# Optimization experiments

Measured on AMD Instinct MI355X. Metric: run time of the kernel, lower is better.

## Reference

```python
import jax, jax.numpy as jnp
import numpy as np

B, T, F_IN, H = 128, 512, 128, 128
EPS = 1e-5


def setup_inputs() -> dict:
    key = jax.random.key(0)
    ks = jax.random.split(key, 24)
    s = 0.05
    r = lambda k, shp: jax.random.normal(k, shp, jnp.float32) * s
    return {
        "x": jax.random.normal(ks[0], (B, T, F_IN), jnp.float32),
        "group_labels": jax.random.randint(ks[1], (B,), 0, 4),
        "conv1_w": r(ks[2], (64, F_IN, 3)), "conv1_b": jnp.zeros((64,), jnp.float32),
        "bn1_g": jnp.ones((64,), jnp.float32), "bn1_b": jnp.zeros((64,), jnp.float32),
        "conv2_w": r(ks[3], (128, 64, 3)), "conv2_b": jnp.zeros((128,), jnp.float32),
        "bn2_g": jnp.ones((128,), jnp.float32), "bn2_b": jnp.zeros((128,), jnp.float32),
        "wih0": r(ks[4], (2, 4 * H, 128)), "whh0": r(ks[5], (2, 4 * H, H)), "b0": r(ks[6], (2, 4 * H)),
        "wih1": r(ks[7], (2, 4 * H, 2 * H)), "whh1": r(ks[8], (2, 4 * H, H)), "b1": r(ks[9], (2, 4 * H)),
        "att_w": r(ks[10], (2 * H,)), "att_b": r(ks[11], (1,)),
        "dec_w1": r(ks[12], (4, 64, 2 * H)), "dec_b1": r(ks[13], (4, 64)),
        "dec_w2": r(ks[14], (4, 32, 64)), "dec_b2": r(ks[15], (4, 32)),
        "dec_w3": r(ks[16], (4, 1, 32)), "dec_b3": r(ks[17], (4, 1)),
    }


def _bn(x, g, b):
    # training-mode batch stats over (N, L) per channel; x: (B, C, L)
    m = x.mean(axis=(0, 2), keepdims=True)
    v = x.var(axis=(0, 2), keepdims=True)
    return (x - m) / jnp.sqrt(v + EPS) * g[None, :, None] + b[None, :, None]


def _conv1d(x, w, b):
    # x: (B, C, L), w: (O, I, 3), padding=1
    y = jax.lax.conv_general_dilated(x, w, (1,), ((1, 1),), dimension_numbers=("NCH", "OIH", "NCH"))
    return y + b[None, :, None]


def _lstm_dir(x, wih, whh, b, reverse):
    Bv, Hv = x.shape[0], whh.shape[1]
    xg = jnp.einsum("btd,gd->btg", x, wih) + b  # precomputed input gates (B, T, 4H)

    def step(carry, xt):
        h, c = carry
        gates = xt + h @ whh.T
        i, f, g, o = jnp.split(gates, 4, axis=-1)  # torch gate order i,f,g,o
        c = jax.nn.sigmoid(f) * c + jax.nn.sigmoid(i) * jnp.tanh(g)
        h = jax.nn.sigmoid(o) * jnp.tanh(c)
        return (h, c), h

    init = (jnp.zeros((Bv, Hv), x.dtype), jnp.zeros((Bv, Hv), x.dtype))
    _, hs = jax.lax.scan(step, init, jnp.swapaxes(xg, 0, 1), reverse=reverse)
    return jnp.swapaxes(hs, 0, 1)  # (B, T, H), time-aligned for both directions


def _bilstm(x, wih, whh, b):
    hf = _lstm_dir(x, wih[0], whh[0], b[0], False)
    hb = _lstm_dir(x, wih[1], whh[1], b[1], True)
    return jnp.concatenate([hf, hb], axis=-1)


def reference(x, group_labels, conv1_w, conv1_b, bn1_g, bn1_b, conv2_w, conv2_b,
              bn2_g, bn2_b, wih0, whh0, b0, wih1, whh1, b1, att_w, att_b,
              dec_w1, dec_b1, dec_w2, dec_b2, dec_w3, dec_b3):
    # ---- shared encoder ----
    h = jnp.swapaxes(x, 1, 2)                          # (B, F, T)
    h = jax.nn.relu(_bn(_conv1d(h, conv1_w, conv1_b), bn1_g, bn1_b))
    h = jax.nn.relu(_bn(_conv1d(h, conv2_w, conv2_b), bn2_g, bn2_b))
    h = jnp.swapaxes(h, 1, 2)                          # (B, T, 128)
    h = _bilstm(h, wih0, whh0, b0)                     # (B, T, 2H)
    h = _bilstm(h, wih1, whh1, b1)                     # (B, T, 2H)
    scores = h @ att_w + att_b                         # (B, T)
    attn = jax.nn.softmax(scores, axis=1)
    attended = jnp.einsum("bt,btd->bd", attn, h)       # (B, 2H)
    # ---- group-routed decoders (batch=1 per sample in original => BN skipped) ----
    h1 = jax.nn.relu(jnp.einsum("bd,ehd->beh", attended, dec_w1) + dec_b1[None])   # (B,4,64)
    h2 = jax.nn.relu(jnp.einsum("beh,egh->beg", h1, dec_w2) + dec_b2[None])         # (B,4,32)
    outs = jnp.einsum("beg,eog->beo", h2, dec_w3) + dec_b3[None]                    # (B,4,1)
    preds = jnp.take_along_axis(outs[:, :, 0], group_labels[:, None], axis=1)       # (B,1)
    return preds, attn
```

## Files before the change

### kernel.cpp

```cpp
#include <hip/hip_runtime.h>
#include <hip/hip_bf16.h>

#define EPS_ 1e-5f

typedef __attribute__((ext_vector_type(4))) float f32x4;
typedef __attribute__((ext_vector_type(8))) short s16x8;
typedef __attribute__((ext_vector_type(4))) short s16x4;
typedef unsigned short u16;

static __device__ __forceinline__ u16 f2bf(float f) {
  __hip_bfloat16 h = __float2bfloat16(f);
  return *reinterpret_cast<u16*>(&h);
}
static __device__ __forceinline__ float bf2f(u16 u) {
  union { float f; unsigned int i; } v; v.i = ((unsigned int)u) << 16; return v.f;
}
static __device__ __forceinline__ float sigf(float x) {
  return __builtin_amdgcn_rcpf(1.f + __expf(-x));
}
static __device__ __forceinline__ float tanhf_(float x) {
  return 2.f * __builtin_amdgcn_rcpf(1.f + __expf(-2.f * x)) - 1.f;
}
static __device__ __forceinline__ f32x4 mfma16(s16x8 a, s16x8 b, f32x4 c) {
  return __builtin_amdgcn_mfma_f32_16x16x32_bf16(a, b, c, 0, 0, 0);
}

__global__ void convw_kernel(const float* __restrict__ src, u16* __restrict__ dst,
                             int KIN, int ksbits, int total) {
  int i = blockIdx.x * 256 + threadIdx.x;
  if (i >= total) return;
  int e = i & 7;
  int lane = (i >> 3) & 63;
  int w = (i >> 9) & 7;
  int g = (i >> 12) & 3;
  int t2 = i >> 14;
  int ks = t2 & ((1 << ksbits) - 1);
  int d = t2 >> ksbits;
  int r = g * 128 + w * 16 + (lane & 15);
  int k = ks * 32 + (lane >> 4) * 8 + e;
  dst[i] = f2bf(src[((size_t)d * 512 + r) * KIN + k]);
}

__global__ void convwf_kernel(const float* __restrict__ src, u16* __restrict__ dst,
                              int IC, int NW, int total) {
  int i = blockIdx.x * 256 + threadIdx.x;
  if (i >= total) return;
  int e = i & 7;
  int lane = (i >> 3) & 63;
  int blk = i >> 9;
  int wb = blk % NW;
  int ks = blk / NW;
  int oc = wb * 16 + (lane & 15);
  int k = ks * 32 + (lane >> 4) * 8 + e;
  int tap = k / IC;
  int ic = k - tap * IC;
  dst[i] = f2bf(src[(oc * IC + ic) * 3 + tap]);
}

template<int IC, int NW, bool BN>
__global__ __launch_bounds__(512, 1) void convm_kernel(
    const float* __restrict__ xin, const u16* __restrict__ wP,
    const float* __restrict__ bsrc, const float* __restrict__ stats_in,
    const float* __restrict__ g_in, const float* __restrict__ beta_in,
    float* __restrict__ yout, float* __restrict__ stats_out) {
  constexpr int OC = NW * 16;
  constexpr int NKS = (3 * IC) / 32;
  constexpr int ICQ = IC / 32;
  __shared__ u16 xs[66 * IC];
  __shared__ float insc[IC], insh[IC];

  const int tid = threadIdx.x;
  const int wv = tid >> 6, lane = tid & 63, q = lane >> 4, col = lane & 15;
  const int b = blockIdx.x >> 3;
  const int t0 = (blockIdx.x & 7) * 64;
  char* xsb = (char*)xs;

  if constexpr (BN) {
    for (int c = tid; c < IC; c += 512) {
      float s0 = stats_in[2 * c], s1 = stats_in[2 * c + 1];
      float m = s0 * (1.f / 65536.f);
      float v = s1 * (1.f / 65536.f) - m * m;
      float inv = rsqrtf(v + EPS_);
      float a = g_in[c] * inv;
      insc[c] = a; insh[c] = beta_in[c] - m * a;
    }
    __syncthreads();
  }

  for (int n = tid; n < 66 * (IC / 4); n += 512) {
    int r = n / (IC / 4);
    int c4 = (n % (IC / 4)) * 4;
    int t = t0 + r - 1;
    float v0 = 0.f, v1 = 0.f, v2 = 0.f, v3 = 0.f;
    if (t >= 0 && t < 512) {
      f32x4 v = *(const f32x4*)&xin[((size_t)b * 512 + t) * IC + c4];
      v0 = v[0]; v1 = v[1]; v2 = v[2]; v3 = v[3];
      if constexpr (BN) {
        v0 = fmaxf(v0 * insc[c4 + 0] + insh[c4 + 0], 0.f);
        v1 = fmaxf(v1 * insc[c4 + 1] + insh[c4 + 1], 0.f);
        v2 = fmaxf(v2 * insc[c4 + 2] + insh[c4 + 2], 0.f);
        v3 = fmaxf(v3 * insc[c4 + 3] + insh[c4 + 3], 0.f);
      }
    }
    s16x4 u;
    u[0] = (short)f2bf(v0); u[1] = (short)f2bf(v1);
    u[2] = (short)f2bf(v2); u[3] = (short)f2bf(v3);
    int byte = ((r * IC + c4) * 2) ^ ((r & 7) << 4);
    *(s16x4*)(xsb + byte) = u;
  }
  __syncthreads();

  const int wb = (NW == 8) ? wv : (wv & 3);
  const s16x8* wPv = (const s16x8*)wP;
  s16x8 aA[NKS];
#pragma unroll
  for (int ks = 0; ks < NKS; ++ks)
    aA[ks] = wPv[(ks * NW + wb) * 64 + lane];

  f32x4 bias4 = *(const f32x4*)&bsrc[wb * 16 + q * 4];

  constexpr int NSUB = (NW == 8) ? 4 : 2;
  const int st0 = (NW == 8) ? 0 : ((wv >> 2) * 2);

  float ssum0 = 0.f, ssum1 = 0.f, ssum2 = 0.f, ssum3 = 0.f;
  float ssq0 = 0.f, ssq1 = 0.f, ssq2 = 0.f, ssq3 = 0.f;

#pragma unroll
  for (int s = 0; s < NSUB; ++s) {
    const int tbase = (st0 + s) * 16;
    const int t_loc = tbase + col;
    f32x4 acc = bias4;
#pragma unroll
    for (int ks = 0; ks < NKS; ++ks) {
      const int tap = ks / ICQ;
      const int icb = (ks % ICQ) * 32 + q * 8;
      const int R = t_loc + tap;
      int byte = ((R * IC + icb) * 2) ^ ((R & 7) << 4);
      s16x8 bB = *(const s16x8*)(xsb + byte);
      acc = mfma16(aA[ks], bB, acc);
    }
    *(f32x4*)&yout[((size_t)b * 512 + t0 + t_loc) * OC + wb * 16 + q * 4] = acc;
    ssum0 += acc[0]; ssq0 += acc[0] * acc[0];
    ssum1 += acc[1]; ssq1 += acc[1] * acc[1];
    ssum2 += acc[2]; ssq2 += acc[2] * acc[2];
    ssum3 += acc[3]; ssq3 += acc[3] * acc[3];
  }

#define RED16(S)                                   \
  S += __shfl_xor(S, 1, 64); S += __shfl_xor(S, 2, 64); \
  S += __shfl_xor(S, 4, 64); S += __shfl_xor(S, 8, 64);
  RED16(ssum0) RED16(ssum1) RED16(ssum2) RED16(ssum3)
  RED16(ssq0)  RED16(ssq1)  RED16(ssq2)  RED16(ssq3)
#undef RED16
  if (col == 0) {
    const int ocb = wb * 16 + q * 4;
    atomicAdd(&stats_out[2 * (ocb + 0)], ssum0);
    atomicAdd(&stats_out[2 * (ocb + 0) + 1], ssq0);
    atomicAdd(&stats_out[2 * (ocb + 1)], ssum1);
    atomicAdd(&stats_out[2 * (ocb + 1) + 1], ssq1);
    atomicAdd(&stats_out[2 * (ocb + 2)], ssum2);
    atomicAdd(&stats_out[2 * (ocb + 2) + 1], ssq2);
    atomicAdd(&stats_out[2 * (ocb + 3)], ssum3);
    atomicAdd(&stats_out[2 * (ocb + 3) + 1], ssq3);
  }
}

template<int KIN, bool BN>
__global__ __launch_bounds__(512, 1) void xg_kernel(
    const void* __restrict__ xin_, const float* __restrict__ stats,
    const float* __restrict__ bng, const float* __restrict__ bnb,
    const u16* __restrict__ wihP, const float* __restrict__ bias,
    u16* __restrict__ xgo) {
  constexpr int NKS = KIN / 32;
  constexpr int XSTR = KIN + 8;
  __shared__ u16 xl[2][16][XSTR];
  __shared__ float sc[128], sh[128];

  const int tid = threadIdx.x;
  const int wv = tid >> 6, lane = tid & 63, q = lane >> 4, col = lane & 15;
  const int bid = blockIdx.x;
  const int dir = bid >> 7, bg = (bid >> 4) & 7, t0 = (bid & 15) * 32;
  const int b0 = bg * 16;
  const int ss = tid >> 5, cc = tid & 31;
  const float* xf = (const float*)xin_;
  const u16* xh = (const u16*)xin_;

  if constexpr (BN) {
    for (int c = tid; c < 128; c += 512) {
      float s0 = stats[2 * c], s1 = stats[2 * c + 1];
      float m = s0 * (1.f / 65536.f);
      float v = s1 * (1.f / 65536.f) - m * m;
      float inv = rsqrtf(v + EPS_);
      float a = bng[c] * inv;
      sc[c] = a; sh[c] = bnb[c] - m * a;
    }
    __syncthreads();
  }

  const s16x8* wihv = (const s16x8*)wihP;
  s16x8 aw[NKS][4];
#pragma unroll
  for (int ks = 0; ks < NKS; ++ks)
#pragma unroll
    for (int g = 0; g < 4; ++g)
      aw[ks][g] = wihv[(((dir * NKS + ks) * 4 + g) * 8 + wv) * 64 + lane];

  f32x4 bias4[4];
#pragma unroll
  for (int g = 0; g < 4; ++g)
    bias4[g] = *(const f32x4*)&bias[dir * 512 + g * 128 + wv * 16 + q * 4];

  if constexpr (KIN == 128) {
    f32x4 v = *(const f32x4*)&xf[((size_t)(b0 + ss) * 512 + t0) * 128 + cc * 4];
    s16x4 u;
#pragma unroll
    for (int j = 0; j < 4; ++j) {
      float xx = v[j];
      if constexpr (BN) xx = fmaxf(xx * sc[cc * 4 + j] + sh[cc * 4 + j], 0.f);
      u[j] = (short)f2bf(xx);
    }
    *(s16x4*)&xl[0][ss][cc * 4] = u;
  } else {
    *(s16x8*)&xl[0][ss][cc * 8] =
        *(const s16x8*)&xh[((size_t)(b0 + ss) * 512 + t0) * 256 + cc * 8];
  }
  __syncthreads();

  int cur = 0;
  for (int i = 0; i < 32; ++i) {
    const int t = t0 + i;
    const int tn = t0 + ((i < 31) ? i + 1 : 31);
    f32x4 xnf; s16x8 xnh;
    if constexpr (KIN == 128)
      xnf = *(const f32x4*)&xf[((size_t)(b0 + ss) * 512 + tn) * 128 + cc * 4];
    else
      xnh = *(const s16x8*)&xh[((size_t)(b0 + ss) * 512 + tn) * 256 + cc * 8];

    s16x8 bx[NKS];
#pragma unroll
    for (int ks = 0; ks < NKS; ++ks)
      bx[ks] = *(const s16x8*)&xl[cur][col][ks * 32 + q * 8];

    f32x4 a0 = bias4[0], a1 = bias4[1], a2 = bias4[2], a3 = bias4[3];
#pragma unroll
    for (int ks = 0; ks < NKS; ++ks) {
      a0 = mfma16(aw[ks][0], bx[ks], a0);
      a1 = mfma16(aw[ks][1], bx[ks], a1);
      a2 = mfma16(aw[ks][2], bx[ks], a2);
      a3 = mfma16(aw[ks][3], bx[ks], a3);
    }

    u16* op = xgo + (((size_t)((dir * 8 + bg) * 512 + t)) * 32 + wv * 4) * 256
            + (size_t)lane * 4;
#define STORE_G(G, A)                                              \
    { s16x4 o;                                                     \
      o[0] = (short)f2bf(A[0]); o[1] = (short)f2bf(A[1]);          \
      o[2] = (short)f2bf(A[2]); o[3] = (short)f2bf(A[3]);          \
      *(s16x4*)(op + G * 256) = o; }
    STORE_G(0, a0) STORE_G(1, a1) STORE_G(2, a2) STORE_G(3, a3)
#undef STORE_G

    if constexpr (KIN == 128) {
      s16x4 u;
#pragma unroll
      for (int j = 0; j < 4; ++j) {
        float xx = xnf[j];
        if constexpr (BN) xx = fmaxf(xx * sc[cc * 4 + j] + sh[cc * 4 + j], 0.f);
        u[j] = (short)f2bf(xx);
      }
      *(s16x4*)&xl[cur ^ 1][ss][cc * 4] = u;
    } else {
      *(s16x8*)&xl[cur ^ 1][ss][cc * 8] = xnh;
    }
    __syncthreads();
    cur ^= 1;
  }
}

__global__ __launch_bounds__(512, 1) void lstm_kernel(
    const u16* __restrict__ whhP, const u16* __restrict__ xg,
    u16* __restrict__ hout) {
  __shared__ u16 hl[2][16][136];
  const int tid = threadIdx.x;
  const int wv = tid >> 6, lane = tid & 63, q = lane >> 4, col = lane & 15;
  const int dir = blockIdx.x >> 3, bg = blockIdx.x & 7, b0 = bg * 16;

  for (int n = tid; n < 16 * 136; n += 512) (&hl[0][0][0])[n] = 0;

  const s16x8* whhv = (const s16x8*)whhP;
  s16x8 awhh[4][4];
#pragma unroll
  for (int ks = 0; ks < 4; ++ks)
#pragma unroll
    for (int g = 0; g < 4; ++g)
      awhh[ks][g] = whhv[(((dir * 4 + ks) * 4 + g) * 8 + wv) * 64 + lane];

  const u16* xgp = xg + ((size_t)(dir * 8 + bg)) * 512 * 8192
                 + (size_t)(wv * 4) * 256 + (size_t)lane * 4;

  const int tstep = dir ? -1 : 1;
  int t = dir ? 511 : 0;

  s16x4 xn0 = *(const s16x4*)(xgp + (size_t)t * 8192);
  s16x4 xn1 = *(const s16x4*)(xgp + (size_t)t * 8192 + 256);
  s16x4 xn2 = *(const s16x4*)(xgp + (size_t)t * 8192 + 512);
  s16x4 xn3 = *(const s16x4*)(xgp + (size_t)t * 8192 + 768);

  __syncthreads();

  float c0 = 0.f, c1 = 0.f, c2 = 0.f, c3 = 0.f;
  int cur = 0;

  for (int it = 0; it < 512; ++it) {
    s16x4 xc0 = xn0, xc1 = xn1, xc2 = xn2, xc3 = xn3;
    const int tn = (it < 511) ? t + tstep : t;
    xn0 = *(const s16x4*)(xgp + (size_t)tn * 8192);
    xn1 = *(const s16x4*)(xgp + (size_t)tn * 8192 + 256);
    xn2 = *(const s16x4*)(xgp + (size_t)tn * 8192 + 512);
    xn3 = *(const s16x4*)(xgp + (size_t)tn * 8192 + 768);

    s16x8 bh[4];
#pragma unroll
    for (int ks = 0; ks < 4; ++ks)
      bh[ks] = *(const s16x8*)&hl[cur][col][ks * 32 + q * 8];

    f32x4 a0, a1, a2, a3;
#pragma unroll
    for (int e = 0; e < 4; ++e) {
      a0[e] = bf2f((u16)xc0[e]); a1[e] = bf2f((u16)xc1[e]);
      a2[e] = bf2f((u16)xc2[e]); a3[e] = bf2f((u16)xc3[e]);
    }
#pragma unroll
    for (int ks = 0; ks < 4; ++ks) {
      a0 = mfma16(awhh[ks][0], bh[ks], a0);
      a1 = mfma16(awhh[ks][1], bh[ks], a1);
      a2 = mfma16(awhh[ks][2], bh[ks], a2);
      a3 = mfma16(awhh[ks][3], bh[ks], a3);
    }

    f32x4 hn;
#define GATE_STEP(E, CP)                                            \
    {                                                               \
      float sI = sigf(a0[E]); float sF = sigf(a1[E]);               \
      float tG = tanhf_(a2[E]); float sO = sigf(a3[E]);             \
      float cn = sF * CP + sI * tG;                                 \
      CP = cn;                                                      \
      hn[E] = sO * tanhf_(cn);                                      \
    }
    GATE_STEP(0, c0) GATE_STEP(1, c1) GATE_STEP(2, c2) GATE_STEP(3, c3)
#undef GATE_STEP

    s16x4 hb;
#pragma unroll
    for (int e = 0; e < 4; ++e) hb[e] = (short)f2bf(hn[e]);
    *(s16x4*)&hout[((size_t)(b0 + col) * 512 + t) * 256 + dir * 128 + wv * 16 + q * 4] = hb;
    *(s16x4*)&hl[cur ^ 1][col][wv * 16 + q * 4] = hb;

    asm volatile("s_waitcnt lgkmcnt(0)" ::: "memory");
    __builtin_amdgcn_sched_barrier(0);
    __builtin_amdgcn_s_barrier();
    __builtin_amdgcn_sched_barrier(0);

    cur ^= 1;
    t += tstep;
  }
}

__global__ __launch_bounds__(256) void attn_kernel(
    const u16* __restrict__ h1, const float* __restrict__ attw,
    const float* __restrict__ attb, float* __restrict__ out_attn,
    float* __restrict__ attended) {
  const int b = blockIdx.x;
  const int tid = threadIdx.x;
  const int w = tid >> 6, l = tid & 63;
  __shared__ float sl[512];
  __shared__ float red[256];
  __shared__ float red2[4][256];

  f32x4 wv4 = *(const f32x4*)&attw[l * 4];
  const float ab = attb[0];
  for (int i = 0; i < 128; ++i) {
    int t = w * 128 + i;
    s16x4 v = *(const s16x4*)&h1[((size_t)b * 512 + t) * 256 + l * 4];
    float s = bf2f((u16)v[0]) * wv4[0] + bf2f((u16)v[1]) * wv4[1]
            + bf2f((u16)v[2]) * wv4[2] + bf2f((u16)v[3]) * wv4[3];
#pragma unroll
    for (int m = 32; m > 0; m >>= 1) s += __shfl_xor(s, m, 64);
    if (l == 0) sl[t] = s + ab;
  }
  __syncthreads();

  red[tid] = fmaxf(sl[tid], sl[tid + 256]);
  __syncthreads();
  for (int st = 128; st > 0; st >>= 1) {
    if (tid < st) red[tid] = fmaxf(red[tid], red[tid + st]);
    __syncthreads();
  }
  const float mx = red[0];
  __syncthreads();

  float e0 = __expf(sl[tid] - mx);
  float e1 = __expf(sl[tid + 256] - mx);
  sl[tid] = e0; sl[tid + 256] = e1;
  red[tid] = e0 + e1;
  __syncthreads();
  for (int st = 128; st > 0; st >>= 1) {
    if (tid < st) red[tid] += red[tid + st];
    __syncthreads();
  }
  const float inv = 1.f / red[0];

  out_attn[(size_t)b * 512 + tid] = sl[tid] * inv;
  out_attn[(size_t)b * 512 + tid + 256] = sl[tid + 256] * inv;
  __syncthreads();

  float a0 = 0.f, a1 = 0.f, a2 = 0.f, a3 = 0.f;
  for (int i = 0; i < 128; ++i) {
    int t = w * 128 + i;
    float p = sl[t] * inv;
    s16x4 v = *(const s16x4*)&h1[((size_t)b * 512 + t) * 256 + l * 4];
    a0 += p * bf2f((u16)v[0]); a1 += p * bf2f((u16)v[1]);
    a2 += p * bf2f((u16)v[2]); a3 += p * bf2f((u16)v[3]);
  }
  red2[w][l * 4 + 0] = a0; red2[w][l * 4 + 1] = a1;
  red2[w][l * 4 + 2] = a2; red2[w][l * 4 + 3] = a3;
  __syncthreads();
  attended[b * 256 + tid] =
      red2[0][tid] + red2[1][tid] + red2[2][tid] + red2[3][tid];
}

__global__ __launch_bounds__(64) void dec_kernel(
    const float* __restrict__ attended, const int* __restrict__ labels,
    const float* __restrict__ w1, const float* __restrict__ b1,
    const float* __restrict__ w2, const float* __restrict__ b2,
    const float* __restrict__ w3, const float* __restrict__ b3,
    float* __restrict__ preds) {
  const int b = blockIdx.x;
  const int tid = threadIdx.x;
  const int g = labels[b];
  __shared__ float al[256];
  __shared__ float hl1[64];
  __shared__ float hl2[32];

  for (int i = tid; i < 256; i += 64) al[i] = attended[b * 256 + i];
  __syncthreads();

  {
    const float* wr = &w1[(size_t)(g * 64 + tid) * 256];
    float a = b1[g * 64 + tid];
    for (int d = 0; d < 256; d += 4) {
      f32x4 wv = *(const f32x4*)&wr[d];
      a += al[d] * wv[0] + al[d + 1] * wv[1] + al[d + 2] * wv[2] + al[d + 3] * wv[3];
    }
    hl1[tid] = fmaxf(a, 0.f);
  }
  __syncthreads();
  if (tid < 32) {
    const float* wr = &w2[(size_t)(g * 32 + tid) * 64];
    float a = b2[g * 32 + tid];
    for (int d = 0; d < 64; d += 4) {
      f32x4 wv = *(const f32x4*)&wr[d];
      a += hl1[d] * wv[0] + hl1[d + 1] * wv[1] + hl1[d + 2] * wv[2] + hl1[d + 3] * wv[3];
    }
    hl2[tid] = fmaxf(a, 0.f);
  }
  __syncthreads();
  if (tid < 32) {
    float a = hl2[tid] * w3[g * 32 + tid];
#pragma unroll
    for (int m = 16; m > 0; m >>= 1) a += __shfl_xor(a, m, 32);
    if (tid == 0) preds[b] = a + b3[g];
  }
}

extern "C" void kernel_launch(void* const* d_in, const int* in_sizes, int n_in,
                              void* d_out, int out_size, void* d_ws, size_t ws_size,
                              hipStream_t stream) {
  const float* x      = (const float*)d_in[0];
  const int*   labels = (const int*)d_in[1];
  const float* conv1w = (const float*)d_in[2];
  const float* conv1b = (const float*)d_in[3];
  const float* bn1g   = (const float*)d_in[4];
  const float* bn1b   = (const float*)d_in[5];
  const float* conv2w = (const float*)d_in[6];
  const float* conv2b = (const float*)d_in[7];
  const float* bn2g   = (const float*)d_in[8];
  const float* bn2b   = (const float*)d_in[9];
  const float* wih0   = (const float*)d_in[10];
  const float* whh0   = (const float*)d_in[11];
  const float* b0     = (const float*)d_in[12];
  const float* wih1   = (const float*)d_in[13];
  const float* whh1   = (const float*)d_in[14];
  const float* b1     = (const float*)d_in[15];
  const float* attw   = (const float*)d_in[16];
  const float* attb   = (const float*)d_in[17];
  const float* dw1    = (const float*)d_in[18];
  const float* db1    = (const float*)d_in[19];
  const float* dw2    = (const float*)d_in[20];
  const float* db2    = (const float*)d_in[21];
  const float* dw3    = (const float*)d_in[22];
  const float* db3    = (const float*)d_in[23];

  char* ws = (char*)d_ws;
  u16*   whh0P = (u16*)  (ws + 0x000000);
  u16*   whh1P = (u16*)  (ws + 0x040000);
  u16*   wih0P = (u16*)  (ws + 0x080000);
  u16*   wih1P = (u16*)  (ws + 0x0C0000);
  u16*   cw1P  = (u16*)  (ws + 0x140000);
  u16*   cw2P  = (u16*)  (ws + 0x150000);
  float* st1   = (float*)(ws + 0x170000);
  float* st2   = (float*)(ws + 0x170200);
  float* attd  = (float*)(ws + 0x170600);
  u16*   h0    = (u16*)  (ws + 0x200000);
  float* y2    = (float*)(ws + 0x2200000);
  u16*   h1    = (u16*)  (ws + 0x2200000);
  u16*   xgb   = (u16*)  (ws + 0x4200000);
  float* y1    = (float*)(ws + 0x4200000);

  float* preds    = (float*)d_out;
  float* attn_out = (float*)d_out + 128;

  hipMemsetAsync(ws + 0x170000, 0, 0x600, stream);

  convw_kernel<<<512, 256, 0, stream>>>(wih0, wih0P, 128, 2, 131072);
  convw_kernel<<<512, 256, 0, stream>>>(whh0, whh0P, 128, 2, 131072);
  convw_kernel<<<1024, 256, 0, stream>>>(wih1, wih1P, 256, 3, 262144);
  convw_kernel<<<512, 256, 0, stream>>>(whh1, whh1P, 128, 2, 131072);
  convwf_kernel<<<96, 256, 0, stream>>>(conv1w, cw1P, 128, 4, 24576);
  convwf_kernel<<<96, 256, 0, stream>>>(conv2w, cw2P, 64, 8, 24576);

  convm_kernel<128, 4, false><<<1024, 512, 0, stream>>>(
      x, cw1P, conv1b, nullptr, nullptr, nullptr, y1, st1);
  convm_kernel<64, 8, true><<<1024, 512, 0, stream>>>(
      y1, cw2P, conv2b, st1, bn1g, bn1b, y2, st2);

  xg_kernel<128, true><<<256, 512, 0, stream>>>(
      y2, st2, bn2g, bn2b, wih0P, b0, xgb);
  lstm_kernel<<<16, 512, 0, stream>>>(whh0P, xgb, h0);
  xg_kernel<256, false><<<256, 512, 0, stream>>>(
      h0, nullptr, nullptr, nullptr, wih1P, b1, xgb);
  lstm_kernel<<<16, 512, 0, stream>>>(whh1P, xgb, h1);

  attn_kernel<<<128, 256, 0, stream>>>(h1, attw, attb, attn_out, attd);
  dec_kernel<<<128, 64, 0, stream>>>(attd, labels, dw1, db1, dw2, db2, dw3, db3, preds);
}
```

Baseline: 1.752 ms.

## Rewrite LSTM recurrence as one-sequence-per-block fp16 dot2 with register-resident weights

Replaces the 16-block MFMA LSTM with 256 blocks, each handling one sequence, where each thread owns one hidden unit and holds its four Whh gate rows in registers as fp16, computing gates with packed dot2 instructions. The input-gate producer now writes gates interleaved per unit per chain so each thread reads four gates with one load. This spreads the serial recurrence across far more compute units to cut per-step latency from the small grid. It risks heavy register pressure, a long dependent dot-product chain per step, and different rounding from fp16 weights and hidden state.

```diff
diff --git a/kernel.cpp b/kernel.cpp
--- a/kernel.cpp
+++ b/kernel.cpp
@@ -6,6 +6,8 @@
 typedef __attribute__((ext_vector_type(4))) float f32x4;
 typedef __attribute__((ext_vector_type(8))) short s16x8;
 typedef __attribute__((ext_vector_type(4))) short s16x4;
+typedef _Float16 h16x2 __attribute__((ext_vector_type(2)));
+typedef _Float16 h16x8 __attribute__((ext_vector_type(8)));
 typedef unsigned short u16;
 
 static __device__ __forceinline__ u16 f2bf(float f) {
@@ -23,6 +25,13 @@
 }
 static __device__ __forceinline__ f32x4 mfma16(s16x8 a, s16x8 b, f32x4 c) {
   return __builtin_amdgcn_mfma_f32_16x16x32_bf16(a, b, c, 0, 0, 0);
+}
+static __device__ __forceinline__ float dot2(h16x2 a, h16x2 b, float c) {
+#if __has_builtin(__builtin_amdgcn_fdot2)
+  return __builtin_amdgcn_fdot2(a, b, c, false);
+#else
+  return fmaf((float)a[0], (float)b[0], fmaf((float)a[1], (float)b[1], c));
+#endif
 }
 
 __global__ void convw_kernel(const float* __restrict__ src, u16* __restrict__ dst,
@@ -41,6 +50,18 @@
   dst[i] = f2bf(src[((size_t)d * 512 + r) * KIN + k]);
 }
 
+__global__ void whhd_kernel(const float* __restrict__ src, _Float16* __restrict__ dst,
+                            int total) {
+  int i = blockIdx.x * 256 + threadIdx.x;
+  if (i >= total) return;
+  int e = i & 7;
+  int u = (i >> 3) & 127;
+  int jo = (i >> 10) & 15;
+  int g = (i >> 14) & 3;
+  int d = i >> 16;
+  dst[i] = (_Float16)src[((size_t)d * 512 + g * 128 + u) * 128 + jo * 8 + e];
+}
+
 __global__ void convwf_kernel(const float* __restrict__ src, u16* __restrict__ dst,
                               int IC, int NW, int total) {
   int i = blockIdx.x * 256 + threadIdx.x;
@@ -127,8 +148,7 @@
 
 #pragma unroll
   for (int s = 0; s < NSUB; ++s) {
-    const int tbase = (st0 + s) * 16;
-    const int t_loc = tbase + col;
+    const int t_loc = (st0 + s) * 16 + col;
     f32x4 acc = bias4;
 #pragma unroll
     for (int ks = 0; ks < NKS; ++ks) {
@@ -226,6 +246,7 @@
   }
   __syncthreads();
 
+  const size_t chain = (size_t)dir * 128 + b0 + col;
   int cur = 0;
   for (int i = 0; i < 32; ++i) {
     const int t = t0 + i;
@@ -250,15 +271,18 @@
       a3 = mfma16(aw[ks][3], bx[ks], a3);
     }
 
-    u16* op = xgo + (((size_t)((dir * 8 + bg) * 512 + t)) * 32 + wv * 4) * 256
-            + (size_t)lane * 4;
-#define STORE_G(G, A)                                              \
-    { s16x4 o;                                                     \
-      o[0] = (short)f2bf(A[0]); o[1] = (short)f2bf(A[1]);          \
-      o[2] = (short)f2bf(A[2]); o[3] = (short)f2bf(A[3]);          \
-      *(s16x4*)(op + G * 256) = o; }
-    STORE_G(0, a0) STORE_G(1, a1) STORE_G(2, a2) STORE_G(3, a3)
-#undef STORE_G
+    u16* op = xgo + (chain * 512 + (size_t)t) * 512 + (size_t)(wv * 16 + q * 4) * 4;
+    s16x8 lo, hi;
+    lo[0] = (short)f2bf(a0[0]); lo[1] = (short)f2bf(a1[0]);
+    lo[2] = (short)f2bf(a2[0]); lo[3] = (short)f2bf(a3[0]);
+    lo[4] = (short)f2bf(a0[1]); lo[5] = (short)f2bf(a1[1]);
+    lo[6] = (short)f2bf(a2[1]); lo[7] = (short)f2bf(a3[1]);
+    hi[0] = (short)f2bf(a0[2]); hi[1] = (short)f2bf(a1[2]);
+    hi[2] = (short)f2bf(a2[2]); hi[3] = (short)f2bf(a3[2]);
+    hi[4] = (short)f2bf(a0[3]); hi[5] = (short)f2bf(a1[3]);
+    hi[6] = (short)f2bf(a2[3]); hi[7] = (short)f2bf(a3[3]);
+    *(s16x8*)op = lo;
+    *(s16x8*)(op + 8) = hi;
 
     if constexpr (KIN == 128) {
       s16x4 u;
@@ -277,84 +301,80 @@
   }
 }
 
-__global__ __launch_bounds__(512, 1) void lstm_kernel(
-    const u16* __restrict__ whhP, const u16* __restrict__ xg,
+__global__ __launch_bounds__(128, 1) void lstm2_kernel(
+    const _Float16* __restrict__ whhD, const u16* __restrict__ xg2,
     u16* __restrict__ hout) {
-  __shared__ u16 hl[2][16][136];
-  const int tid = threadIdx.x;
-  const int wv = tid >> 6, lane = tid & 63, q = lane >> 4, col = lane & 15;
-  const int dir = blockIdx.x >> 3, bg = blockIdx.x & 7, b0 = bg * 16;
-
-  for (int n = tid; n < 16 * 136; n += 512) (&hl[0][0][0])[n] = 0;
-
-  const s16x8* whhv = (const s16x8*)whhP;
-  s16x8 awhh[4][4];
-#pragma unroll
-  for (int ks = 0; ks < 4; ++ks)
-#pragma unroll
-    for (int g = 0; g < 4; ++g)
-      awhh[ks][g] = whhv[(((dir * 4 + ks) * 4 + g) * 8 + wv) * 64 + lane];
-
-  const u16* xgp = xg + ((size_t)(dir * 8 + bg)) * 512 * 8192
-                 + (size_t)(wv * 4) * 256 + (size_t)lane * 4;
-
+  __shared__ _Float16 hl[2][128];
+  const int u = threadIdx.x;
+  const int dir = blockIdx.x >> 7, s = blockIdx.x & 127;
+  const size_t chain = (size_t)dir * 128 + s;
+
+  const h16x8* wv8 = (const h16x8*)whhD;
+  h16x2 w0[64], w1[64], w2[64], w3[64];
+#pragma unroll
+  for (int jo = 0; jo < 16; ++jo) {
+    union { h16x8 v; h16x2 h[4]; } t0u, t1u, t2u, t3u;
+    t0u.v = wv8[((dir * 4 + 0) * 16 + jo) * 128 + u];
+    t1u.v = wv8[((dir * 4 + 1) * 16 + jo) * 128 + u];
+    t2u.v = wv8[((dir * 4 + 2) * 16 + jo) * 128 + u];
+    t3u.v = wv8[((dir * 4 + 3) * 16 + jo) * 128 + u];
+#pragma unroll
+    for (int p = 0; p < 4; ++p) {
+      w0[jo * 4 + p] = t0u.h[p];
+      w1[jo * 4 + p] = t1u.h[p];
+      w2[jo * 4 + p] = t2u.h[p];
+      w3[jo * 4 + p] = t3u.h[p];
+    }
+  }
+
+  hl[0][u] = (_Float16)0.f;
+
+  const u16* xp = xg2 + chain * 512 * 512 + (size_t)u * 4;
   const int tstep = dir ? -1 : 1;
   int t = dir ? 511 : 0;
 
-  s16x4 xn0 = *(const s16x4*)(xgp + (size_t)t * 8192);
-  s16x4 xn1 = *(const s16x4*)(xgp + (size_t)t * 8192 + 256);
-  s16x4 xn2 = *(const s16x4*)(xgp + (size_t)t * 8192 + 512);
-  s16x4 xn3 = *(const s16x4*)(xgp + (size_t)t * 8192 + 768);
-
-  __syncthreads();
-
-  float c0 = 0.f, c1 = 0.f, c2 = 0.f, c3 = 0.f;
+  s16x4 xn = *(const s16x4*)(xp + (size_t)t * 512);
+
+  __syncthreads();
+
+  float c = 0.f;
   int cur = 0;
 
   for (int it = 0; it < 512; ++it) {
-    s16x4 xc0 = xn0, xc1 = xn1, xc2 = xn2, xc3 = xn3;
+    s16x4 xc = xn;
     const int tn = (it < 511) ? t + tstep : t;
-    xn0 = *(const s16x4*)(xgp + (size_t)tn * 8192);
-    xn1 = *(const s16x4*)(xgp + (size_t)tn * 8192 + 256);
-    xn2 = *(const s16x4*)(xgp + (size_t)tn * 8192 + 512);
-    xn3 = *(const s16x4*)(xgp + (size_t)tn * 8192 + 768);
-
-    s16x8 bh[4];
-#pragma unroll
-    for (int ks = 0; ks < 4; ++ks)
-      bh[ks] = *(const s16x8*)&hl[cur][col][ks * 32 + q * 8];
-
-    f32x4 a0, a1, a2, a3;
-#pragma unroll
-    for (int e = 0; e < 4; ++e) {
-      a0[e] = bf2f((u16)xc0[e]); a1[e] = bf2f((u16)xc1[e]);
-      a2[e] = bf2f((u16)xc2[e]); a3[e] = bf2f((u16)xc3[e]);
-    }
-#pragma unroll
-    for (int ks = 0; ks < 4; ++ks) {
-      a0 = mfma16(awhh[ks][0], bh[ks], a0);
-      a1 = mfma16(awhh[ks][1], bh[ks], a1);
-      a2 = mfma16(awhh[ks][2], bh[ks], a2);
-      a3 = mfma16(awhh[ks][3], bh[ks], a3);
-    }
-
-    f32x4 hn;
-#define GATE_STEP(E, CP)                                            \
-    {                                                               \
-      float sI = sigf(a0[E]); float sF = sigf(a1[E]);               \
-      float tG = tanhf_(a2[E]); float sO = sigf(a3[E]);             \
-      float cn = sF * CP + sI * tG;                                 \
-      CP = cn;                                                      \
-      hn[E] = sO * tanhf_(cn);                                      \
-    }
-    GATE_STEP(0, c0) GATE_STEP(1, c1) GATE_STEP(2, c2) GATE_STEP(3, c3)
-#undef GATE_STEP
-
-    s16x4 hb;
-#pragma unroll
-    for (int e = 0; e < 4; ++e) hb[e] = (short)f2bf(hn[e]);
-    *(s16x4*)&hout[((size_t)(b0 + col) * 512 + t) * 256 + dir * 128 + wv * 16 + q * 4] = hb;
-    *(s16x4*)&hl[cur ^ 1][col][wv * 16 + q * 4] = hb;
+    xn = *(const s16x4*)(xp + (size_t)tn * 512);
+
+    h16x2 hh[64];
+#pragma unroll
+    for (int jo = 0; jo < 16; ++jo) {
+      union { h16x8 v; h16x2 h[4]; } th;
+      th.v = *(const h16x8*)&hl[cur][jo * 8];
+#pragma unroll
+      for (int p = 0; p < 4; ++p) hh[jo * 4 + p] = th.h[p];
+    }
+
+    float ai = bf2f((u16)xc[0]), af = bf2f((u16)xc[1]);
+    float ag = bf2f((u16)xc[2]), ao = bf2f((u16)xc[3]);
+    float pi = 0.f, pf = 0.f, pg = 0.f, po = 0.f;
+#pragma unroll
+    for (int j = 0; j < 64; ++j) {
+      if (j & 1) {
+        pi = dot2(hh[j], w0[j], pi); pf = dot2(hh[j], w1[j], pf);
+        pg = dot2(hh[j], w2[j], pg); po = dot2(hh[j], w3[j], po);
+      } else {
+        ai = dot2(hh[j], w0[j], ai); af = dot2(hh[j], w1[j], af);
+        ag = dot2(hh[j], w2[j], ag); ao = dot2(hh[j], w3[j], ao);
+      }
+    }
+    ai += pi; af += pf; ag += pg; ao += po;
+
+    float sI = sigf(ai), sF = sigf(af), tG = tanhf_(ag), sO = sigf(ao);
+    c = sF * c + sI * tG;
+    float hn = sO * tanhf_(c);
+
+    hout[((size_t)s * 512 + t) * 256 + dir * 128 + u] = f2bf(hn);
+    hl[cur ^ 1][u] = (_Float16)hn;
 
     asm volatile("s_waitcnt lgkmcnt(0)" ::: "memory");
     __builtin_amdgcn_sched_barrier(0);
@@ -502,8 +522,8 @@
   const float* db3    = (const float*)d_in[23];
 
   char* ws = (char*)d_ws;
-  u16*   whh0P = (u16*)  (ws + 0x000000);
-  u16*   whh1P = (u16*)  (ws + 0x040000);
+  _Float16* whhD0 = (_Float16*)(ws + 0x000000);
+  _Float16* whhD1 = (_Float16*)(ws + 0x040000);
   u16*   wih0P = (u16*)  (ws + 0x080000);
   u16*   wih1P = (u16*)  (ws + 0x0C0000);
   u16*   cw1P  = (u16*)  (ws + 0x140000);
@@ -520,12 +540,12 @@
   float* preds    = (float*)d_out;
   float* attn_out = (float*)d_out + 128;
 
-  hipMemsetAsync(ws + 0x170000, 0, 0x600, stream);
+  (void)hipMemsetAsync(ws + 0x170000, 0, 0x600, stream);
 
   convw_kernel<<<512, 256, 0, stream>>>(wih0, wih0P, 128, 2, 131072);
-  convw_kernel<<<512, 256, 0, stream>>>(whh0, whh0P, 128, 2, 131072);
   convw_kernel<<<1024, 256, 0, stream>>>(wih1, wih1P, 256, 3, 262144);
-  convw_kernel<<<512, 256, 0, stream>>>(whh1, whh1P, 128, 2, 131072);
+  whhd_kernel<<<512, 256, 0, stream>>>(whh0, whhD0, 131072);
+  whhd_kernel<<<512, 256, 0, stream>>>(whh1, whhD1, 131072);
   convwf_kernel<<<96, 256, 0, stream>>>(conv1w, cw1P, 128, 4, 24576);
   convwf_kernel<<<96, 256, 0, stream>>>(conv2w, cw2P, 64, 8, 24576);
 
@@ -536,10 +556,10 @@
 
   xg_kernel<128, true><<<256, 512, 0, stream>>>(
       y2, st2, bn2g, bn2b, wih0P, b0, xgb);
-  lstm_kernel<<<16, 512, 0, stream>>>(whh0P, xgb, h0);
+  lstm2_kernel<<<256, 128, 0, stream>>>(whhD0, xgb, h0);
   xg_kernel<256, false><<<256, 512, 0, stream>>>(
       h0, nullptr, nullptr, nullptr, wih1P, b1, xgb);
-  lstm_kernel<<<16, 512, 0, stream>>>(whh1P, xgb, h1);
+  lstm2_kernel<<<256, 128, 0, stream>>>(whhD1, xgb, h1);
 
   attn_kernel<<<128, 256, 0, stream>>>(h1, attw, attb, attn_out, attd);
   dec_kernel<<<128, 64, 0, stream>>>(attd, labels, dw1, db1, dw2, db2, dw3, db3, preds);
```

After: 2.156 ms. 1.23x slower.
